# Kernel tuning notes

Measured on AMD Instinct MI355X. Metric: run time of the kernel, lower is better.

The kernel has to match this reference:

```python
import jax, jax.numpy as jnp
import numpy as np

N, G, P = 512, 11560, 2000
E_SG, E_GP, E_PP = 1000000, 200000, 50000
HID, HEADS, L = 192, 4, 2
C = HID // HEADS
NQ, OUT = 20, 128
EPS = 1e-5


def setup_inputs():
    key = jax.random.key(0)
    ks = iter(jax.random.split(key, 64))
    def rn(shape, s=0.05):
        return jax.random.normal(next(ks), shape, jnp.float32) * s
    def ri(n, hi):
        return jax.random.randint(next(ks), (n,), 0, hi)
    return dict(
        x_sample=rn((N, HID), 1.0), x_gene=rn((G, HID), 1.0), x_pathway=rn((P, HID), 1.0),
        e_sg_src=ri(E_SG, N), e_sg_dst=ri(E_SG, G),
        e_gp_src=ri(E_GP, G), e_gp_dst=ri(E_GP, P),
        e_pp_src=ri(E_PP, P), e_pp_dst=ri(E_PP, P),
        sage_Wl=rn((L, 2, HID, HID)), sage_bl=jnp.zeros((L, 2, HID)), sage_Wr=rn((L, 2, HID, HID)),
        gat_Wl=rn((L, 3, HID, HID)), gat_bl=jnp.zeros((L, 3, HID)),
        gat_Wr=rn((L, 3, HID, HID)), gat_br=jnp.zeros((L, 3, HID)),
        gat_att=rn((L, 3, HEADS, C), 0.1), gat_bias=jnp.zeros((L, 3, HID)),
        ln_g=jnp.ones((L, 3, HID)), ln_b=jnp.zeros((L, 3, HID)),
        pool_query=rn((NQ, HID), 1.0),
        pool_in_w=rn((3 * HID, HID)), pool_in_b=jnp.zeros((3 * HID,)),
        pool_out_w=rn((HID, HID)), pool_out_b=jnp.zeros((HID,)),
        ff_w1=rn((HID, HID)), ff_b1=jnp.zeros((HID,)),
        ff_w2=rn((HID, HID)), ff_b2=jnp.zeros((HID,)),
        pool_ln_g=jnp.ones((HID,)), pool_ln_b=jnp.zeros((HID,)),
        proj_w=rn((OUT, HID)), proj_b=jnp.zeros((OUT,)),
    )


def _ln(x, g, b):
    mu = x.mean(-1, keepdims=True)
    v = ((x - mu) ** 2).mean(-1, keepdims=True)
    return (x - mu) / jnp.sqrt(v + EPS) * g + b


def _sage(x_src, x_dst, src, dst, Wl, bl, Wr, n_dst):
    # PyG SAGEConv: lin_l(mean_aggr(x_src[neighbors])) + lin_r(x_dst)
    s = jax.ops.segment_sum(x_src[src], dst, num_segments=n_dst)
    cnt = jax.ops.segment_sum(jnp.ones((src.shape[0],), x_src.dtype), dst, num_segments=n_dst)
    mean = s / jnp.maximum(cnt, 1.0)[:, None]
    return mean @ Wl.T + bl + x_dst @ Wr.T


def _gatv2(x_src, x_dst, src, dst, Wl, bl, Wr, br, att, bias, n_dst):
    # transform nodes first (cheap), then gather per edge
    gl = (x_src @ Wl.T + bl).reshape(-1, HEADS, C)[src]   # [E,H,C]
    gr = (x_dst @ Wr.T + br).reshape(-1, HEADS, C)[dst]   # [E,H,C]
    e = jax.nn.leaky_relu(gl + gr, 0.2)
    score = jnp.einsum('ehc,hc->eh', e, att)              # [E,H]
    m = jax.ops.segment_max(score, dst, num_segments=n_dst)
    ex = jnp.exp(score - m[dst])
    den = jax.ops.segment_sum(ex, dst, num_segments=n_dst)
    alpha = ex / (den[dst] + 1e-16)
    out = jax.ops.segment_sum(alpha[:, :, None] * gl, dst, num_segments=n_dst)
    return out.reshape(n_dst, HID) + bias


def reference(x_sample, x_gene, x_pathway, e_sg_src, e_sg_dst, e_gp_src, e_gp_dst,
              e_pp_src, e_pp_dst, sage_Wl, sage_bl, sage_Wr, gat_Wl, gat_bl, gat_Wr,
              gat_br, gat_att, gat_bias, ln_g, ln_b, pool_query, pool_in_w, pool_in_b,
              pool_out_w, pool_out_b, ff_w1, ff_b1, ff_w2, ff_b2, pool_ln_g, pool_ln_b,
              proj_w, proj_b):
    xs, xg, xp = x_sample, x_gene, x_pathway
    for l in range(L):
        og = _sage(xs, xg, e_sg_src, e_sg_dst, sage_Wl[l, 0], sage_bl[l, 0], sage_Wr[l, 0], G)
        os_ = _sage(xg, xs, e_sg_dst, e_sg_src, sage_Wl[l, 1], sage_bl[l, 1], sage_Wr[l, 1], N)
        op = _gatv2(xg, xp, e_gp_src, e_gp_dst, gat_Wl[l, 0], gat_bl[l, 0], gat_Wr[l, 0],
                    gat_br[l, 0], gat_att[l, 0], gat_bias[l, 0], P)
        og = og + _gatv2(xp, xg, e_gp_dst, e_gp_src, gat_Wl[l, 1], gat_bl[l, 1], gat_Wr[l, 1],
                         gat_br[l, 1], gat_att[l, 1], gat_bias[l, 1], G)
        op = op + _gatv2(xp, xp, e_pp_src, e_pp_dst, gat_Wl[l, 2], gat_bl[l, 2], gat_Wr[l, 2],
                         gat_br[l, 2], gat_att[l, 2], gat_bias[l, 2], P)
        # residual + LayerNorm (dropout = identity in eval)
        xs = _ln(xs + os_, ln_g[l, 0], ln_b[l, 0])
        xg = _ln(xg + og, ln_g[l, 1], ln_b[l, 1])
        xp = _ln(xp + op, ln_g[l, 2], ln_b[l, 2])
    # MultiQueryPooling over sample nodes (batch=1 MultiheadAttention)
    Wq, Wk, Wv = jnp.split(pool_in_w, 3, axis=0)
    bq, bk, bv = jnp.split(pool_in_b, 3, axis=0)
    q = (pool_query @ Wq.T + bq).reshape(NQ, HEADS, C)
    k = (xs @ Wk.T + bk).reshape(N, HEADS, C)
    v = (xs @ Wv.T + bv).reshape(N, HEADS, C)
    attn = jax.nn.softmax(jnp.einsum('qhc,nhc->hqn', q, k) / (C ** 0.5), axis=-1)
    o = jnp.einsum('hqn,nhc->qhc', attn, v).reshape(NQ, HID) @ pool_out_w.T + pool_out_b
    pooled = o.mean(0)  # [HID]
    h = jax.nn.relu(pooled @ ff_w1.T + ff_b1) @ ff_w2.T + ff_b2
    h = _ln(h, pool_ln_g, pool_ln_b)
    return (h @ proj_w.T + proj_b)[None, :]  # [1, OUT]
```

## Files before the change

### kernel.cpp

```cpp
#include <hip/hip_runtime.h>

#define N_S 512
#define N_G 11560
#define N_P 2000
#define NE_SG 1000000
#define NE_GP 200000
#define NE_PP 50000
#define HID 192
#define HEADS 4
#define CDIM 48
#define NQd 20
#define OUTD 128
#define LDK 12288
#define SPLITK 16
#define CHUNKK 768

typedef __attribute__((ext_vector_type(8))) short short8;
typedef __attribute__((ext_vector_type(4))) float float4v;

__device__ __forceinline__ float bf2f(unsigned short u){
  union { unsigned int i; float f; } x; x.i = ((unsigned int)u) << 16; return x.f;
}
__device__ __forceinline__ unsigned short f2bf(float f){
  union { float f; unsigned int i; } u; u.f = f;
  unsigned int r = u.i + 0x7FFFu + ((u.i >> 16) & 1u);
  return (unsigned short)(r >> 16);
}
__device__ __forceinline__ ushort4 f4bf(float4 v){
  return make_ushort4(f2bf(v.x), f2bf(v.y), f2bf(v.z), f2bf(v.w));
}

__global__ __launch_bounds__(256) void k_detect(const unsigned int* __restrict__ raw,
                                                int* __restrict__ flag){
  __shared__ int cnt;
  if (threadIdx.x == 0) cnt = 0;
  __syncthreads();
  int c = 0;
  for (int i = threadIdx.x; i < 2048; i += 256) {
    float f = __uint_as_float(raw[i]);
    float a = fabsf(f);
    if (f == f && a > 1e-4f && a < 1000.0f) c++;
  }
  atomicAdd(&cnt, c);
  __syncthreads();
  if (threadIdx.x == 0) flag[0] = (cnt >= 1024) ? 1 : 0;
}

#define NLOAD 27
#define LOADBX 2048
struct LoadDesc { const void* src; float* dst; int n; };
struct LoadTable { LoadDesc d[NLOAD]; };
__global__ __launch_bounds__(256)
void k_load_all(LoadTable tab, const int* __restrict__ flag){
  LoadDesc de = tab.d[blockIdx.y];
  int fp32 = flag[0];
  for (int i = blockIdx.x*256 + threadIdx.x; i < de.n; i += LOADBX*256) {
    if (fp32) de.dst[i] = ((const float*)de.src)[i];
    else      de.dst[i] = bf2f(((const unsigned short*)de.src)[i]);
  }
}

__global__ __launch_bounds__(256)
void k_cntbuild(const int* __restrict__ src, const int* __restrict__ dst,
                int* __restrict__ cg, int E){
  int i = blockIdx.x*256 + threadIdx.x;
  if (i >= E) return;
  atomicAdd(&cg[(size_t)dst[i]*N_S + src[i]], 1);
}

__global__ __launch_bounds__(256)
void k_cvtT(const int* __restrict__ cg, unsigned short* __restrict__ bfA,
            unsigned short* __restrict__ bfB){
  __shared__ unsigned short tile[64][68];
  int g0 = blockIdx.x*64, s0 = blockIdx.y*64;
  int t = threadIdx.x; int r = t>>2, seg = t&3;
  int g = g0 + r;
  if (g < N_G) {
    const int* row = cg + (size_t)g*N_S + s0 + seg*16;
    unsigned short* arow = bfA + (size_t)g*N_S + s0 + seg*16;
    #pragma unroll
    for (int i=0;i<16;i++){
      unsigned short v = f2bf((float)row[i]);
      tile[r][seg*16+i] = v;
      arow[i] = v;
    }
  } else {
    #pragma unroll
    for (int i=0;i<16;i++) tile[r][seg*16+i] = 0;
  }
  __syncthreads();
  int s = s0 + r;
  unsigned short* brow = bfB + (size_t)s*LDK + g0 + seg*16;
  #pragma unroll
  for (int i=0;i<16;i++) brow[i] = tile[seg*16+i][r];
}

__global__ __launch_bounds__(256)
void k_rowinv_i(const int* __restrict__ A, int lda, int cols, int n,
                float* __restrict__ outp){
  int row = blockIdx.x*4 + (threadIdx.x >> 6);
  if (row >= n) return;
  int lane = threadIdx.x & 63;
  const int* Ar = A + (size_t)row*lda;
  float s = 0.0f;
  for (int c = lane; c < cols; c += 64) s += (float)Ar[c];
  #pragma unroll
  for (int o = 32; o; o >>= 1) s += __shfl_xor(s, o);
  if (lane == 0) outp[row] = 1.0f / fmaxf(s, 1.0f);
}
__global__ __launch_bounds__(256)
void k_rowinv_h(const unsigned short* __restrict__ A, int lda, int cols, int n,
                float* __restrict__ outp){
  int row = blockIdx.x;
  if (row >= n) return;
  int t = threadIdx.x;
  const short8* Av = (const short8*)(A + (size_t)row*lda);
  float s = 0.0f;
  for (int i = t; i < cols/8; i += 256) {
    short8 v = Av[i];
    #pragma unroll
    for (int j = 0; j < 8; j++) s += bf2f((unsigned short)v[j]);
  }
  #pragma unroll
  for (int o = 32; o; o >>= 1) s += __shfl_xor(s, o);
  __shared__ float red[4];
  int w = t >> 6, lane = t & 63;
  if (lane == 0) red[w] = s;
  __syncthreads();
  if (t == 0) {
    float tot = red[0] + red[1] + red[2] + red[3];
    outp[row] = 1.0f / fmaxf(tot, 1.0f);
  }
}

struct TransJobs { const float* inA; unsigned short* outA; int nA; int ldoA; int rbA;
                   const float* inB; unsigned short* outB; int nB; int ldoB; };
__global__ __launch_bounds__(256)
void k_transpose2(TransJobs tj){
  const float* in; unsigned short* outp; int n, ldo, r0;
  int bx = blockIdx.x;
  if (bx < tj.rbA) { in = tj.inA; outp = tj.outA; n = tj.nA; ldo = tj.ldoA; r0 = bx*64; }
  else             { in = tj.inB; outp = tj.outB; n = tj.nB; ldo = tj.ldoB; r0 = (bx - tj.rbA)*64; }
  __shared__ float tile[64][65];
  int c0 = blockIdx.y*64;
  int t = threadIdx.x;
  int r = t >> 2, seg = t & 3;
  int grr = r0 + r;
  if (grr < n) {
    #pragma unroll
    for (int i = 0; i < 4; i++) {
      float4 v = *(const float4*)(in + (size_t)grr*HID + c0 + seg*16 + i*4);
      tile[r][seg*16+i*4+0] = v.x; tile[r][seg*16+i*4+1] = v.y;
      tile[r][seg*16+i*4+2] = v.z; tile[r][seg*16+i*4+3] = v.w;
    }
  } else {
    #pragma unroll
    for (int i = 0; i < 16; i++) tile[r][seg*16+i] = 0.0f;
  }
  __syncthreads();
  int w = t >> 6, lane = t & 63;
  if (r0 + lane < ldo) {
    #pragma unroll
    for (int j = 0; j < 16; j++) {
      int c = w*16 + j;
      outp[(size_t)(c0+c)*ldo + r0 + lane] = f2bf(tile[lane][c]);
    }
  }
}

struct CsrJob { const int* src; const int* dst; int E; int n;
                int* deg; int* rowptr; int* cursor; int* col; };
struct CsrJobs { CsrJob j[3]; };

__global__ __launch_bounds__(256) void k_hist3(CsrJobs jobs){
  CsrJob jb = jobs.j[blockIdx.y];
  int i = blockIdx.x*256 + threadIdx.x;
  if (i < jb.E) atomicAdd(&jb.deg[jb.dst[i]], 1);
}
__global__ __launch_bounds__(256) void k_scan3(CsrJobs jobs){
  CsrJob jb = jobs.j[blockIdx.x];
  __shared__ int part[256];
  __shared__ int pre[256];
  int t = threadIdx.x;
  int n = jb.n;
  int C = (n + 255) >> 8;
  int lo = t*C, hi = min(n, lo + C);
  int s = 0;
  for (int i = lo; i < hi; i++) s += jb.deg[i];
  part[t] = s;
  __syncthreads();
  if (t == 0) {
    int acc = 0;
    for (int i = 0; i < 256; i++) { pre[i] = acc; acc += part[i]; }
    jb.rowptr[n] = acc;
  }
  __syncthreads();
  int run = pre[t];
  for (int i = lo; i < hi; i++) {
    jb.rowptr[i] = run; jb.cursor[i] = run; run += jb.deg[i];
  }
}
__global__ __launch_bounds__(256) void k_fill3(CsrJobs jobs){
  CsrJob jb = jobs.j[blockIdx.y];
  int i = blockIdx.x*256 + threadIdx.x;
  if (i >= jb.E) return;
  int pos = atomicAdd(&jb.cursor[jb.dst[i]], 1);
  jb.col[pos] = jb.src[i];
}

#define LDA 200
__global__ __launch_bounds__(256)
void k_gemm(const float* __restrict__ A,
            const float* __restrict__ W, const float* __restrict__ bias,
            float* __restrict__ outp, int n)
{
  __shared__ __align__(16) unsigned short Asm[64*LDA];
  __shared__ __align__(16) unsigned short Wsm[64*LDA];
  int t = threadIdx.x;
  int row0 = blockIdx.x * 64;
  int col0 = blockIdx.y * 64;
  {
    int r = t >> 2, seg = t & 3;
    int gr = row0 + r;
    unsigned short* ad = Asm + r*LDA + seg*48;
    if (gr < n) {
      const float* Ar = A + (size_t)gr*HID + seg*48;
      #pragma unroll
      for (int i = 0; i < 12; i++) {
        float4 v = *reinterpret_cast<const float4*>(Ar + i*4);
        *reinterpret_cast<ushort4*>(ad + i*4) = f4bf(v);
      }
    } else {
      ushort4 z = make_ushort4(0,0,0,0);
      #pragma unroll
      for (int i = 0; i < 12; i++) *reinterpret_cast<ushort4*>(ad + i*4) = z;
    }
    const float* Wr = W + (size_t)(col0 + r)*HID + seg*48;
    unsigned short* wd = Wsm + r*LDA + seg*48;
    #pragma unroll
    for (int i = 0; i < 12; i++) {
      float4 v = *reinterpret_cast<const float4*>(Wr + i*4);
      *reinterpret_cast<ushort4*>(wd + i*4) = f4bf(v);
    }
  }
  __syncthreads();
  int w = t >> 6, lane = t & 63;
  int quad = lane >> 4, mr = lane & 15;
  float4v acc[4] = {};
  const unsigned short* Abase = Asm + (w*16 + mr)*LDA + quad*8;
  const unsigned short* Wbase = Wsm + mr*LDA + quad*8;
  #pragma unroll
  for (int k0 = 0; k0 < 6; k0++) {
    short8 a = *reinterpret_cast<const short8*>(Abase + k0*32);
    #pragma unroll
    for (int ct = 0; ct < 4; ct++) {
      short8 b = *reinterpret_cast<const short8*>(Wbase + ct*16*LDA + k0*32);
      acc[ct] = __builtin_amdgcn_mfma_f32_16x16x32_bf16(a, b, acc[ct], 0, 0, 0);
    }
  }
  #pragma unroll
  for (int ct = 0; ct < 4; ct++) {
    #pragma unroll
    for (int reg = 0; reg < 4; reg++) {
      int rr = row0 + w*16 + quad*4 + reg;
      if (rr < n) {
        int cc = col0 + ct*16 + mr;
        outp[(size_t)rr*HID + cc] = acc[ct][reg] + bias[cc];
      }
    }
  }
}

struct GemmJob { const float* A; const float* W; const float* bias;
                 unsigned short* out; int n; };
struct GemmJobs { GemmJob j[6]; int rb[7]; };
__global__ __launch_bounds__(256)
void k_gemm6(GemmJobs jobs)
{
  int bx = blockIdx.x;
  int z = 0;
  #pragma unroll
  for (int q = 1; q < 6; q++) if (bx >= jobs.rb[q]) z = q;
  GemmJob jb = jobs.j[z];
  int row0 = (bx - jobs.rb[z]) * 64;
  __shared__ __align__(16) unsigned short Asm[64*LDA];
  __shared__ __align__(16) unsigned short Wsm[64*LDA];
  int t = threadIdx.x;
  int col0 = blockIdx.y * 64;
  {
    int r = t >> 2, seg = t & 3;
    int gr = row0 + r;
    unsigned short* ad = Asm + r*LDA + seg*48;
    if (gr < jb.n) {
      const float* Ar = jb.A + (size_t)gr*HID + seg*48;
      #pragma unroll
      for (int i = 0; i < 12; i++) {
        float4 v = *reinterpret_cast<const float4*>(Ar + i*4);
        *reinterpret_cast<ushort4*>(ad + i*4) = f4bf(v);
      }
    } else {
      ushort4 zz = make_ushort4(0,0,0,0);
      #pragma unroll
      for (int i = 0; i < 12; i++) *reinterpret_cast<ushort4*>(ad + i*4) = zz;
    }
    const float* Wr = jb.W + (size_t)(col0 + r)*HID + seg*48;
    unsigned short* wd = Wsm + r*LDA + seg*48;
    #pragma unroll
    for (int i = 0; i < 12; i++) {
      float4 v = *reinterpret_cast<const float4*>(Wr + i*4);
      *reinterpret_cast<ushort4*>(wd + i*4) = f4bf(v);
    }
  }
  __syncthreads();
  int w = t >> 6, lane = t & 63;
  int quad = lane >> 4, mr = lane & 15;
  float4v acc[4] = {};
  const unsigned short* Abase = Asm + (w*16 + mr)*LDA + quad*8;
  const unsigned short* Wbase = Wsm + mr*LDA + quad*8;
  #pragma unroll
  for (int k0 = 0; k0 < 6; k0++) {
    short8 a = *reinterpret_cast<const short8*>(Abase + k0*32);
    #pragma unroll
    for (int ct = 0; ct < 4; ct++) {
      short8 b = *reinterpret_cast<const short8*>(Wbase + ct*16*LDA + k0*32);
      acc[ct] = __builtin_amdgcn_mfma_f32_16x16x32_bf16(a, b, acc[ct], 0, 0, 0);
    }
  }
  #pragma unroll
  for (int ct = 0; ct < 4; ct++) {
    #pragma unroll
    for (int reg = 0; reg < 4; reg++) {
      int rr = row0 + w*16 + quad*4 + reg;
      if (rr < jb.n) {
        int cc = col0 + ct*16 + mr;
        jb.out[(size_t)rr*HID + cc] = f2bf(acc[ct][reg] + jb.bias[cc]);
      }
    }
  }
}

struct PoolJob { const float* A; const float* W; const float* bias;
                 float* out; int n; };
struct PoolJobs { PoolJob j[3]; int rb[4]; };
__global__ __launch_bounds__(256)
void k_gemm3(PoolJobs jobs)
{
  int bx = blockIdx.x;
  int z = 0;
  if (bx >= jobs.rb[1]) z = 1;
  if (bx >= jobs.rb[2]) z = 2;
  PoolJob jb = jobs.j[z];
  int row0 = (bx - jobs.rb[z]) * 64;
  __shared__ __align__(16) unsigned short Asm[64*LDA];
  __shared__ __align__(16) unsigned short Wsm[64*LDA];
  int t = threadIdx.x;
  int col0 = blockIdx.y * 64;
  {
    int r = t >> 2, seg = t & 3;
    int gr = row0 + r;
    unsigned short* ad = Asm + r*LDA + seg*48;
    if (gr < jb.n) {
      const float* Ar = jb.A + (size_t)gr*HID + seg*48;
      #pragma unroll
      for (int i = 0; i < 12; i++) {
        float4 v = *reinterpret_cast<const float4*>(Ar + i*4);
        *reinterpret_cast<ushort4*>(ad + i*4) = f4bf(v);
      }
    } else {
      ushort4 zz = make_ushort4(0,0,0,0);
      #pragma unroll
      for (int i = 0; i < 12; i++) *reinterpret_cast<ushort4*>(ad + i*4) = zz;
    }
    const float* Wr = jb.W + (size_t)(col0 + r)*HID + seg*48;
    unsigned short* wd = Wsm + r*LDA + seg*48;
    #pragma unroll
    for (int i = 0; i < 12; i++) {
      float4 v = *reinterpret_cast<const float4*>(Wr + i*4);
      *reinterpret_cast<ushort4*>(wd + i*4) = f4bf(v);
    }
  }
  __syncthreads();
  int w = t >> 6, lane = t & 63;
  int quad = lane >> 4, mr = lane & 15;
  float4v acc[4] = {};
  const unsigned short* Abase = Asm + (w*16 + mr)*LDA + quad*8;
  const unsigned short* Wbase = Wsm + mr*LDA + quad*8;
  #pragma unroll
  for (int k0 = 0; k0 < 6; k0++) {
    short8 a = *reinterpret_cast<const short8*>(Abase + k0*32);
    #pragma unroll
    for (int ct = 0; ct < 4; ct++) {
      short8 b = *reinterpret_cast<const short8*>(Wbase + ct*16*LDA + k0*32);
      acc[ct] = __builtin_amdgcn_mfma_f32_16x16x32_bf16(a, b, acc[ct], 0, 0, 0);
    }
  }
  #pragma unroll
  for (int ct = 0; ct < 4; ct++) {
    #pragma unroll
    for (int reg = 0; reg < 4; reg++) {
      int rr = row0 + w*16 + quad*4 + reg;
      if (rr < jb.n) {
        int cc = col0 + ct*16 + mr;
        jb.out[(size_t)rr*HID + cc] = acc[ct][reg] + jb.bias[cc];
      }
    }
  }
}

struct G2Job { const float* A1; const float* rs1; const float* W1;
               const float* A2; const float* W2; const float* bias;
               float* out; int n; };
struct G2Jobs { G2Job j[2]; int rb[3]; };
__global__ __launch_bounds__(256)
void k_gemm2(G2Jobs jobs)
{
  int bx = blockIdx.x;
  int z = (bx >= jobs.rb[1]) ? 1 : 0;
  G2Job jb = jobs.j[z];
  int row0 = (bx - jobs.rb[z]) * 64;
  __shared__ __align__(16) unsigned short Asm[64*LDA];
  __shared__ __align__(16) unsigned short Wsm[64*LDA];
  int t = threadIdx.x;
  int col0 = blockIdx.y * 64;
  int r = t >> 2, seg = t & 3;
  int w = t >> 6, lane = t & 63;
  int quad = lane >> 4, mr = lane & 15;
  float4v acc[4] = {};
  for (int p = 0; p < 2; p++) {
    if (p) __syncthreads();
    const float* A = p ? jb.A2 : jb.A1;
    const float* W = p ? jb.W2 : jb.W1;
    {
      int gr = row0 + r;
      unsigned short* ad = Asm + r*LDA + seg*48;
      if (gr < jb.n) {
        float sc = (!p && jb.rs1) ? jb.rs1[gr] : 1.0f;
        const float* Ar = A + (size_t)gr*HID + seg*48;
        #pragma unroll
        for (int i = 0; i < 12; i++) {
          float4 v = *reinterpret_cast<const float4*>(Ar + i*4);
          v.x *= sc; v.y *= sc; v.z *= sc; v.w *= sc;
          *reinterpret_cast<ushort4*>(ad + i*4) = f4bf(v);
        }
      } else {
        ushort4 zz = make_ushort4(0,0,0,0);
        #pragma unroll
        for (int i = 0; i < 12; i++) *reinterpret_cast<ushort4*>(ad + i*4) = zz;
      }
      const float* Wr = W + (size_t)(col0 + r)*HID + seg*48;
      unsigned short* wd = Wsm + r*LDA + seg*48;
      #pragma unroll
      for (int i = 0; i < 12; i++) {
        float4 v = *reinterpret_cast<const float4*>(Wr + i*4);
        *reinterpret_cast<ushort4*>(wd + i*4) = f4bf(v);
      }
    }
    __syncthreads();
    const unsigned short* Abase = Asm + (w*16 + mr)*LDA + quad*8;
    const unsigned short* Wbase = Wsm + mr*LDA + quad*8;
    #pragma unroll
    for (int k0 = 0; k0 < 6; k0++) {
      short8 a = *reinterpret_cast<const short8*>(Abase + k0*32);
      #pragma unroll
      for (int ct = 0; ct < 4; ct++) {
        short8 b = *reinterpret_cast<const short8*>(Wbase + ct*16*LDA + k0*32);
        acc[ct] = __builtin_amdgcn_mfma_f32_16x16x32_bf16(a, b, acc[ct], 0, 0, 0);
      }
    }
  }
  #pragma unroll
  for (int ct = 0; ct < 4; ct++) {
    #pragma unroll
    for (int reg = 0; reg < 4; reg++) {
      int rr = row0 + w*16 + quad*4 + reg;
      if (rr < jb.n) {
        int cc = col0 + ct*16 + mr;
        jb.out[(size_t)rr*HID + cc] = acc[ct][reg] + jb.bias[cc];
      }
    }
  }
}

#define BKG 128
#define LDG 136
struct KJob { const unsigned short* A; int lda;
              const unsigned short* W; int ldw;
              float* out; int n; int kbeg; int kend; };
struct KJobs { KJob j[17]; int rb[18]; };
__global__ __launch_bounds__(256)
void k_gemm_k(KJobs jobs)
{
  int bx = blockIdx.x;
  int z = 0;
  for (int q = 1; q < 17; q++) if (bx >= jobs.rb[q]) z = q;
  KJob jb = jobs.j[z];
  int row0 = (bx - jobs.rb[z]) * 64;
  __shared__ __align__(16) unsigned short Asm[64*LDG];
  __shared__ __align__(16) unsigned short Wsm[64*LDG];
  int t = threadIdx.x;
  int col0 = blockIdx.y * 64;
  int r = t >> 2, seg = t & 3;
  int w = t >> 6, lane = t & 63;
  int quad = lane >> 4, mr = lane & 15;
  float4v acc[4] = {};
  for (int k0 = jb.kbeg; k0 < jb.kend; k0 += BKG) {
    {
      int gr = row0 + r;
      unsigned short* ad = Asm + r*LDG + seg*32;
      if (gr < jb.n) {
        const unsigned short* Ar = jb.A + (size_t)gr*jb.lda + k0 + seg*32;
        #pragma unroll
        for (int i = 0; i < 4; i++) *(uint4*)(ad + i*8) = *(const uint4*)(Ar + i*8);
      } else {
        uint4 zz = make_uint4(0,0,0,0);
        #pragma unroll
        for (int i = 0; i < 4; i++) *(uint4*)(ad + i*8) = zz;
      }
      const unsigned short* Wr = jb.W + (size_t)(col0 + r)*jb.ldw + k0 + seg*32;
      unsigned short* wd = Wsm + r*LDG + seg*32;
      #pragma unroll
      for (int i = 0; i < 4; i++) *(uint4*)(wd + i*8) = *(const uint4*)(Wr + i*8);
    }
    __syncthreads();
    const unsigned short* Abase = Asm + (w*16 + mr)*LDG + quad*8;
    const unsigned short* Wbase = Wsm + mr*LDG + quad*8;
    #pragma unroll
    for (int kk = 0; kk < 4; kk++) {
      short8 a = *(const short8*)(Abase + kk*32);
      #pragma unroll
      for (int ct = 0; ct < 4; ct++) {
        short8 b = *(const short8*)(Wbase + ct*16*LDG + kk*32);
        acc[ct] = __builtin_amdgcn_mfma_f32_16x16x32_bf16(a, b, acc[ct], 0, 0, 0);
      }
    }
    __syncthreads();
  }
  #pragma unroll
  for (int ct = 0; ct < 4; ct++) {
    #pragma unroll
    for (int reg = 0; reg < 4; reg++) {
      int rr = row0 + w*16 + quad*4 + reg;
      if (rr < jb.n) jb.out[(size_t)rr*HID + col0 + ct*16 + mr] = acc[ct][reg];
    }
  }
}

__global__ __launch_bounds__(256)
void k_reduce_sk(const float* __restrict__ part, float* __restrict__ outp, int n){
  int i = blockIdx.x*256 + threadIdx.x;
  if (i >= n*HID) return;
  float s = 0.0f;
  #pragma unroll
  for (int z = 0; z < SPLITK; z++) s += part[(size_t)z*n*HID + i];
  outp[i] = s;
}

struct GatJob { const unsigned short* gl; const unsigned short* gr;
                const int* rowptr; const int* col;
                const float* att; const float* bias; float* out; int ndst; int accum; };
struct GatJobs { GatJob j[3]; int bo[4]; };

#define GLS_LD 200
__global__ __launch_bounds__(256)
void k_gat_all(GatJobs jobs)
{
  int bx = blockIdx.x;
  int jz = 0;
  if (bx >= jobs.bo[1]) jz = 1;
  if (bx >= jobs.bo[2]) jz = 2;
  GatJob jb = jobs.j[jz];
  int tid = threadIdx.x;
  int w = tid >> 6, lane = tid & 63;
  int dst = (bx - jobs.bo[jz])*4 + w;
  bool active = dst < jb.ndst;
  __shared__ float attS[HID];
  __shared__ float grS[4][HID];
  __shared__ __align__(16) unsigned short glS[4][16][GLS_LD];
  __shared__ float swS[4][4][16];
  __shared__ float fS[4][4];
  __shared__ float lS[4][4];
  if (tid < HID) attS[tid] = jb.att[tid];
  if (active) {
    const unsigned short* grr = jb.gr + (size_t)dst*HID;
    grS[w][lane]     = bf2f(grr[lane]);
    grS[w][lane+64]  = bf2f(grr[lane+64]);
    grS[w][lane+128] = bf2f(grr[lane+128]);
  }
  __syncthreads();
  if (!active) return;

  int h16 = lane >> 4, j16 = lane & 15;
  int start = jb.rowptr[dst], end = jb.rowptr[dst+1];
  float m = -1e30f, l = 0.0f;
  float acc0 = 0.f, acc1 = 0.f, acc2 = 0.f;
  int hd0 = lane/48, hd1 = (lane+64)/48, hd2 = (lane+128)/48;
  const float* attH = attS + h16*CDIM;
  const float* grH  = grS[w] + h16*CDIM;

  for (int c0 = start; c0 < end; c0 += 16) {
    int nc = min(16, end - c0);
    float sc = -1e30f;
    if (j16 < nc) {
      int s = jb.col[c0 + j16];
      const short8* glv = (const short8*)(jb.gl + (size_t)s*HID + h16*CDIM);
      unsigned short* ls = &glS[w][j16][h16*CDIM];
      float a = 0.0f;
      #pragma unroll
      for (int v8 = 0; v8 < 6; v8++) {
        short8 g8 = glv[v8];
        *(short8*)(ls + v8*8) = g8;
        #pragma unroll
        for (int jj = 0; jj < 8; jj++) {
          float v = bf2f((unsigned short)g8[jj]) + grH[v8*8+jj];
          v = v > 0.0f ? v : 0.2f*v;
          a += v * attH[v8*8+jj];
        }
      }
      sc = a;
    }
    float cm = sc;
    cm = fmaxf(cm, __shfl_xor(cm, 1));
    cm = fmaxf(cm, __shfl_xor(cm, 2));
    cm = fmaxf(cm, __shfl_xor(cm, 4));
    cm = fmaxf(cm, __shfl_xor(cm, 8));
    float nm = fmaxf(m, cm);
    float f = __expf(m - nm);
    l *= f;
    float e = (j16 < nc) ? __expf(sc - nm) : 0.0f;
    swS[w][h16][j16] = e;
    float cl = e;
    cl += __shfl_xor(cl, 1);
    cl += __shfl_xor(cl, 2);
    cl += __shfl_xor(cl, 4);
    cl += __shfl_xor(cl, 8);
    l += cl;
    m = nm;
    if (j16 == 0) fS[w][h16] = f;
    acc0 *= fS[w][hd0]; acc1 *= fS[w][hd1]; acc2 *= fS[w][hd2];
    for (int j = 0; j < nc; j++) {
      acc0 += swS[w][hd0][j] * bf2f(glS[w][j][lane]);
      acc1 += swS[w][hd1][j] * bf2f(glS[w][j][lane+64]);
      acc2 += swS[w][hd2][j] * bf2f(glS[w][j][lane+128]);
    }
  }
  if (j16 == 0) lS[w][h16] = l;
  float* od = jb.out + (size_t)dst*HID;
  float v0 = acc0 / (lS[w][hd0] + 1e-16f) + jb.bias[lane];
  float v1 = acc1 / (lS[w][hd1] + 1e-16f) + jb.bias[lane+64];
  float v2 = acc2 / (lS[w][hd2] + 1e-16f) + jb.bias[lane+128];
  if (jb.accum) { v0 += od[lane]; v1 += od[lane+64]; v2 += od[lane+128]; }
  od[lane] = v0; od[lane+64] = v1; od[lane+128] = v2;
}

__global__ __launch_bounds__(64)
void k_ln3(float* __restrict__ xs, const float* __restrict__ osb,
           float* __restrict__ xg, const float* __restrict__ og,
           float* __restrict__ xp, const float* __restrict__ opb,
           const float* __restrict__ op2,
           const float* __restrict__ LNg, const float* __restrict__ LNb, int l)
{
  int r = blockIdx.x;
  float* x; const float* d1; const float* d2 = nullptr; int typ;
  if (r < N_S)            { x = xs + (size_t)r*HID; d1 = osb + (size_t)r*HID; typ = 0; }
  else if (r < N_S + N_G) { int rr = r - N_S; x = xg + (size_t)rr*HID; d1 = og + (size_t)rr*HID; typ = 1; }
  else                    { int rr = r - N_S - N_G; x = xp + (size_t)rr*HID; d1 = opb + (size_t)rr*HID;
                            d2 = op2 + (size_t)rr*HID; typ = 2; }
  const float* g = LNg + (l*3 + typ)*HID;
  const float* b = LNb + (l*3 + typ)*HID;
  int lane = threadIdx.x;
  float v[3]; float sum = 0.0f;
  #pragma unroll
  for (int j=0;j<3;j++){
    int d = j*64 + lane;
    float t = x[d] + d1[d];
    if (d2) t += d2[d];
    v[j] = t; sum += t;
  }
  #pragma unroll
  for (int o=32;o;o>>=1) sum += __shfl_xor(sum, o);
  float mu = sum * (1.0f/HID);
  float var = 0.0f;
  #pragma unroll
  for (int j=0;j<3;j++){ float dd = v[j]-mu; var += dd*dd; }
  #pragma unroll
  for (int o=32;o;o>>=1) var += __shfl_xor(var, o);
  var *= (1.0f/HID);
  float inv = rsqrtf(var + 1e-5f);
  #pragma unroll
  for (int j=0;j<3;j++){
    int d = j*64 + lane;
    x[d] = (v[j]-mu)*inv*g[d] + b[d];
  }
}

__global__ __launch_bounds__(256)
void k_pool_attn(const float* __restrict__ qb, const float* __restrict__ kb,
                 const float* __restrict__ vb, float* __restrict__ ob)
{
  int h = blockIdx.x & 3;
  int q = blockIdx.x >> 2;
  __shared__ float prob[N_S];
  __shared__ float red[256];
  int t = threadIdx.x;
  const float* qrow = qb + (size_t)q*HID + h*CDIM;
  const float scale = 0.14433756729740643f;
  for (int n = t; n < N_S; n += 256) {
    const float* krow = kb + (size_t)n*HID + h*CDIM;
    float s = 0.0f;
    #pragma unroll 8
    for (int c=0;c<CDIM;c++) s += qrow[c]*krow[c];
    prob[n] = s * scale;
  }
  __syncthreads();
  float m = -1e30f;
  for (int n=t;n<N_S;n+=256) m = fmaxf(m, prob[n]);
  red[t] = m; __syncthreads();
  for (int s2=128;s2;s2>>=1){ if (t<s2) red[t]=fmaxf(red[t],red[t+s2]); __syncthreads(); }
  m = red[0]; __syncthreads();
  float sum = 0.0f;
  for (int n=t;n<N_S;n+=256){ float e=__expf(prob[n]-m); prob[n]=e; sum+=e; }
  red[t] = sum; __syncthreads();
  for (int s2=128;s2;s2>>=1){ if (t<s2) red[t]+=red[t+s2]; __syncthreads(); }
  float inv = 1.0f/red[0];
  __syncthreads();
  if (t < CDIM) {
    float acc = 0.0f;
    for (int n=0;n<N_S;n++) acc += prob[n]*vb[(size_t)n*HID + h*CDIM + t];
    ob[(size_t)q*HID + h*CDIM + t] = acc * inv;
  }
}

__global__ __launch_bounds__(192)
void k_tail(const float* __restrict__ ob2,
            const float* ffw1, const float* ffb1,
            const float* ffw2, const float* ffb2,
            const float* lng, const float* lnb,
            const float* pw, const float* pb,
            void* __restrict__ outp, const int* __restrict__ flag)
{
  __shared__ float pooled[HID];
  __shared__ float hh[HID];
  __shared__ float stats[2];
  int t = threadIdx.x;
  float a = 0.0f;
  for (int q=0;q<NQd;q++) a += ob2[q*HID + t];
  pooled[t] = a * (1.0f/NQd);
  __syncthreads();
  float s1 = ffb1[t];
  for (int k=0;k<HID;k++) s1 += pooled[k]*ffw1[t*HID+k];
  hh[t] = fmaxf(s1, 0.0f);
  __syncthreads();
  float s2 = ffb2[t];
  for (int k=0;k<HID;k++) s2 += hh[k]*ffw2[t*HID+k];
  __syncthreads();
  hh[t] = s2;
  __syncthreads();
  if (t == 0) {
    float mu=0.0f; for (int k=0;k<HID;k++) mu += hh[k];
    mu *= (1.0f/HID);
    float v=0.0f; for (int k=0;k<HID;k++){ float d=hh[k]-mu; v+=d*d; }
    v *= (1.0f/HID);
    stats[0]=mu; stats[1]=rsqrtf(v + 1e-5f);
  }
  __syncthreads();
  pooled[t] = (hh[t]-stats[0])*stats[1]*lng[t] + lnb[t];
  __syncthreads();
  if (t < OUTD) {
    float acc = pb[t];
    for (int k=0;k<HID;k++) acc += pooled[k]*pw[t*HID+k];
    if (flag[0]) ((float*)outp)[t] = acc;
    else         ((unsigned short*)outp)[t] = f2bf(acc);
  }
}

extern "C" void kernel_launch(void* const* d_in, const int* in_sizes, int n_in,
                              void* d_out, int out_size, void* d_ws, size_t ws_size,
                              hipStream_t stream)
{
  const int* sg_src = (const int*)d_in[3];
  const int* sg_dst = (const int*)d_in[4];
  const int* gp_src = (const int*)d_in[5];
  const int* gp_dst = (const int*)d_in[6];
  const int* pp_src = (const int*)d_in[7];
  const int* pp_dst = (const int*)d_in[8];

  float* base = (float*)d_ws;
  size_t off = 0;
  auto alloc = [&](size_t nf){ nf = (nf + 3) & ~(size_t)3; float* p = base + off; off += nf; return p; };
  int*   flag = (int*)alloc(4);
  float* xs   = alloc((size_t)N_S*HID);
  float* xg   = alloc((size_t)N_G*HID);
  float* xp   = alloc((size_t)N_P*HID);
  float* qin  = alloc((size_t)NQd*HID);
  float* Wsl  = alloc(2*2*HID*HID); float* bsl = alloc(2*2*HID); float* Wsr = alloc(2*2*HID*HID);
  float* Wgl  = alloc(2*3*HID*HID); float* bgl = alloc(2*3*HID);
  float* Wgr  = alloc(2*3*HID*HID); float* bgr = alloc(2*3*HID);
  float* Agat = alloc(2*3*HEADS*CDIM); float* Bgat = alloc(2*3*HID);
  float* LNg  = alloc(2*3*HID); float* LNb = alloc(2*3*HID);
  float* Pinw = alloc(3*HID*HID); float* Pinb = alloc(3*HID);
  float* Poutw= alloc(HID*HID);   float* Poutb= alloc(HID);
  float* Fw1  = alloc(HID*HID);   float* Fb1  = alloc(HID);
  float* Fw2  = alloc(HID*HID);   float* Fb2  = alloc(HID);
  float* PLg  = alloc(HID);       float* PLb  = alloc(HID);
  float* Pw   = alloc(OUTD*HID);  float* Pb   = alloc(OUTD);
  float* agg  = alloc((size_t)N_G*HID);
  float* aggS = alloc((size_t)N_S*HID);
  float* og   = alloc((size_t)N_G*HID);
  float* osb  = alloc((size_t)N_S*HID);
  float* opb  = alloc((size_t)N_P*HID);
  float* op2  = alloc((size_t)N_P*HID);
  unsigned short* glGb  = (unsigned short*)alloc((size_t)N_G*HID/2);
  unsigned short* grGb  = (unsigned short*)alloc((size_t)N_G*HID/2);
  unsigned short* grP0b = (unsigned short*)alloc((size_t)N_P*HID/2);
  unsigned short* glP1b = (unsigned short*)alloc((size_t)N_P*HID/2);
  unsigned short* glP2b = (unsigned short*)alloc((size_t)N_P*HID/2);
  unsigned short* grP2b = (unsigned short*)alloc((size_t)N_P*HID/2);
  float* qbuf = alloc((size_t)NQd*HID);
  float* kbuf = alloc((size_t)N_S*HID);
  float* vbuf = alloc((size_t)N_S*HID);
  float* obuf = alloc((size_t)NQd*HID);
  float* ob2  = alloc((size_t)NQd*HID);
  int*            CntGi = (int*)alloc((size_t)N_G*N_S);
  unsigned short* CntGb = (unsigned short*)alloc((size_t)N_G*N_S/2);
  unsigned short* CntSb = (unsigned short*)alloc((size_t)N_S*LDK/2);
  unsigned short* xsTb  = (unsigned short*)alloc((size_t)HID*N_S/2);
  unsigned short* xgTb  = (unsigned short*)alloc((size_t)HID*LDK/2);
  float* part = alloc((size_t)SPLITK*N_S*HID);
  float* invdegG = alloc(N_G);
  float* invdegS = alloc(N_S);
  int* degAll = (int*)alloc(2*N_P + N_G + 4);
  int* curAll = (int*)alloc(2*N_P + N_G + 4);
  int* rp_gp_p = (int*)alloc(N_P+2);  int* col_gp_p = (int*)alloc(NE_GP);
  int* rp_gp_g = (int*)alloc(N_G+2);  int* col_gp_g = (int*)alloc(NE_GP);
  int* rp_pp_p = (int*)alloc(N_P+2);  int* col_pp_p = (int*)alloc(NE_PP);
  (void)ws_size; (void)in_sizes; (void)n_in; (void)out_size;

  k_detect<<<1,256,0,stream>>>((const unsigned int*)d_in[0], flag);

  {
    LoadTable tab;
    int k = 0;
    auto add = [&](int i, float* dst, int n){ tab.d[k].src = d_in[i]; tab.d[k].dst = dst; tab.d[k].n = n; k++; };
    add(0,  xs,  N_S*HID);  add(1,  xg,  N_G*HID);  add(2,  xp,  N_P*HID);
    add(9,  Wsl, 2*2*HID*HID); add(10, bsl, 2*2*HID); add(11, Wsr, 2*2*HID*HID);
    add(12, Wgl, 2*3*HID*HID); add(13, bgl, 2*3*HID);
    add(14, Wgr, 2*3*HID*HID); add(15, bgr, 2*3*HID);
    add(16, Agat, 2*3*HEADS*CDIM); add(17, Bgat, 2*3*HID);
    add(18, LNg, 2*3*HID); add(19, LNb, 2*3*HID);
    add(20, qin, NQd*HID);
    add(21, Pinw, 3*HID*HID); add(22, Pinb, 3*HID);
    add(23, Poutw, HID*HID);  add(24, Poutb, HID);
    add(25, Fw1, HID*HID); add(26, Fb1, HID);
    add(27, Fw2, HID*HID); add(28, Fb2, HID);
    add(29, PLg, HID); add(30, PLb, HID);
    add(31, Pw, OUTD*HID); add(32, Pb, OUTD);
    k_load_all<<<dim3(LOADBX, NLOAD),256,0,stream>>>(tab, flag);
  }

  hipMemsetAsync(CntGi, 0, (size_t)N_G*N_S*4, stream);
  hipMemsetAsync(degAll, 0, (size_t)(2*N_P + N_G)*4, stream);
  k_cntbuild<<<(NE_SG+255)/256,256,0,stream>>>(sg_src, sg_dst, CntGi, NE_SG);
  k_cvtT<<<dim3(LDK/64, N_S/64),256,0,stream>>>(CntGi, CntGb, CntSb);
  k_rowinv_i<<<(N_G+3)/4,256,0,stream>>>(CntGi, N_S, N_S, N_G, invdegG);
  k_rowinv_h<<<N_S,256,0,stream>>>(CntSb, LDK, LDK, N_S, invdegS);

  {
    CsrJobs jobs;
    jobs.j[0] = { gp_src, gp_dst, NE_GP, N_P, degAll,           rp_gp_p, curAll,           col_gp_p };
    jobs.j[1] = { gp_dst, gp_src, NE_GP, N_G, degAll+N_P,       rp_gp_g, curAll+N_P,       col_gp_g };
    jobs.j[2] = { pp_src, pp_dst, NE_PP, N_P, degAll+N_P+N_G,   rp_pp_p, curAll+N_P+N_G,   col_pp_p };
    k_hist3<<<dim3((NE_GP+255)/256, 3),256,0,stream>>>(jobs);
    k_scan3<<<3,256,0,stream>>>(jobs);
    k_fill3<<<dim3((NE_GP+255)/256, 3),256,0,stream>>>(jobs);
  }

  const int RB_G = (N_G+63)/64, RB_P = (N_P+63)/64;
  const int GB_P = (N_P+3)/4,  GB_G = (N_G+3)/4;

  for (int l=0; l<2; l++) {
    {
      TransJobs tj;
      tj.inA = xs; tj.outA = xsTb; tj.nA = N_S; tj.ldoA = N_S; tj.rbA = 8;
      tj.inB = xg; tj.outB = xgTb; tj.nB = N_G; tj.ldoB = LDK;
      k_transpose2<<<dim3(8 + LDK/64, 3),256,0,stream>>>(tj);
    }
    {
      KJobs kj;
      kj.j[0] = { CntGb, N_S, xsTb, N_S, agg, N_G, 0, N_S };
      kj.rb[0] = 0; kj.rb[1] = RB_G;
      for (int z = 0; z < SPLITK; z++) {
        kj.j[1+z] = { CntSb, LDK, xgTb, LDK, part + (size_t)z*N_S*HID, N_S,
                      z*CHUNKK, (z+1)*CHUNKK };
        kj.rb[2+z] = kj.rb[1+z] + 8;
      }
      k_gemm_k<<<dim3(kj.rb[17],3),256,0,stream>>>(kj);
    }
    k_reduce_sk<<<(N_S*HID+255)/256,256,0,stream>>>(part, aggS, N_S);
    {
      G2Jobs g2;
      g2.j[0] = { agg,  invdegG, Wsl + (size_t)(l*2+0)*HID*HID,
                  xg, Wsr + (size_t)(l*2+0)*HID*HID, bsl + (l*2+0)*HID, og,  N_G };
      g2.j[1] = { aggS, invdegS, Wsl + (size_t)(l*2+1)*HID*HID,
                  xs, Wsr + (size_t)(l*2+1)*HID*HID, bsl + (l*2+1)*HID, osb, N_S };
      g2.rb[0] = 0; g2.rb[1] = RB_G; g2.rb[2] = RB_G + (N_S+63)/64;
      k_gemm2<<<dim3(g2.rb[2],3),256,0,stream>>>(g2);
    }
    {
      GemmJobs gj;
      int w0 = l*3+0, w1 = l*3+1, w2 = l*3+2;
      gj.j[0] = { xg, Wgl + (size_t)w0*HID*HID, bgl + w0*HID, glGb,  N_G };
      gj.j[1] = { xp, Wgr + (size_t)w0*HID*HID, bgr + w0*HID, grP0b, N_P };
      gj.j[2] = { xp, Wgl + (size_t)w1*HID*HID, bgl + w1*HID, glP1b, N_P };
      gj.j[3] = { xg, Wgr + (size_t)w1*HID*HID, bgr + w1*HID, grGb,  N_G };
      gj.j[4] = { xp, Wgl + (size_t)w2*HID*HID, bgl + w2*HID, glP2b, N_P };
      gj.j[5] = { xp, Wgr + (size_t)w2*HID*HID, bgr + w2*HID, grP2b, N_P };
      int nrb[6] = { RB_G, RB_P, RB_P, RB_G, RB_P, RB_P };
      gj.rb[0] = 0;
      for (int q = 0; q < 6; q++) gj.rb[q+1] = gj.rb[q] + nrb[q];
      k_gemm6<<<dim3(gj.rb[6],3),256,0,stream>>>(gj);
    }
    {
      GatJobs gt;
      int w0 = l*3+0, w1 = l*3+1, w2 = l*3+2;
      gt.j[0] = { glGb,  grP0b, rp_gp_p, col_gp_p, Agat + (size_t)w0*HID, Bgat + (size_t)w0*HID, opb, N_P, 0 };
      gt.j[1] = { glP1b, grGb,  rp_gp_g, col_gp_g, Agat + (size_t)w1*HID, Bgat + (size_t)w1*HID, og,  N_G, 1 };
      gt.j[2] = { glP2b, grP2b, rp_pp_p, col_pp_p, Agat + (size_t)w2*HID, Bgat + (size_t)w2*HID, op2, N_P, 0 };
      gt.bo[0] = 0; gt.bo[1] = GB_P; gt.bo[2] = GB_P + GB_G; gt.bo[3] = GB_P + GB_G + GB_P;
      k_gat_all<<<dim3(gt.bo[3]),256,0,stream>>>(gt);
    }
    k_ln3<<<N_S+N_G+N_P,64,0,stream>>>(xs, osb, xg, og, xp, opb, op2, LNg, LNb, l);
  }

  {
    PoolJobs pj;
    pj.j[0] = { qin, Pinw,                     Pinb,         qbuf, NQd };
    pj.j[1] = { xs,  Pinw + (size_t)HID*HID,   Pinb + HID,   kbuf, N_S };
    pj.j[2] = { xs,  Pinw + (size_t)2*HID*HID, Pinb + 2*HID, vbuf, N_S };
    pj.rb[0] = 0; pj.rb[1] = 1; pj.rb[2] = 1 + (N_S+63)/64; pj.rb[3] = pj.rb[2] + (N_S+63)/64;
    k_gemm3<<<dim3(pj.rb[3],3),256,0,stream>>>(pj);
  }
  k_pool_attn<<<NQd*HEADS,256,0,stream>>>(qbuf, kbuf, vbuf, obuf);
  k_gemm<<<dim3(1,3),256,0,stream>>>(obuf, Poutw, Poutb, ob2, NQd);
  k_tail<<<1,HID,0,stream>>>(ob2, Fw1, Fb1, Fw2, Fb2, PLg, PLb, Pw, Pb, d_out, flag);
}
```

Measured before the change: 638.3 us.

## Keep bf16 shadow copies of node features and vectorize GAT aggregation

The loader and LayerNorm kernels now also write bf16 copies of the node features. The GEMM kernels then read these directly with 16-byte loads instead of loading fp32 and converting on every use, which cuts global read traffic and conversion work in the repeated GEMMs. Separately, the GAT aggregation now has 48 lanes each handle 4 contiguous channels with float4 accumulators and vector loads, replacing 3 strided scalar accumulators per lane. The cost is extra bf16 writes and memory, and a quarter of the lanes sit idle during aggregation.

Measured after the change: 613.0 us. 1.04x faster.

```diff
diff --git a/kernel.cpp b/kernel.cpp
--- a/kernel.cpp
+++ b/kernel.cpp
@@ -48,15 +48,17 @@
 
 #define NLOAD 27
 #define LOADBX 2048
-struct LoadDesc { const void* src; float* dst; int n; };
+struct LoadDesc { const void* src; float* dst; unsigned short* dst16; int n; };
 struct LoadTable { LoadDesc d[NLOAD]; };
 __global__ __launch_bounds__(256)
 void k_load_all(LoadTable tab, const int* __restrict__ flag){
   LoadDesc de = tab.d[blockIdx.y];
   int fp32 = flag[0];
+  unsigned short* m = de.dst16;
   for (int i = blockIdx.x*256 + threadIdx.x; i < de.n; i += LOADBX*256) {
-    if (fp32) de.dst[i] = ((const float*)de.src)[i];
-    else      de.dst[i] = bf2f(((const unsigned short*)de.src)[i]);
+    float v = fp32 ? ((const float*)de.src)[i] : bf2f(((const unsigned short*)de.src)[i]);
+    de.dst[i] = v;
+    if (m) m[i] = f2bf(v);
   }
 }
 
@@ -271,7 +273,7 @@
   }
 }
 
-struct GemmJob { const float* A; const float* W; const float* bias;
+struct GemmJob { const unsigned short* A; const float* W; const float* bias;
                  unsigned short* out; int n; };
 struct GemmJobs { GemmJob j[6]; int rb[7]; };
 __global__ __launch_bounds__(256)
@@ -292,16 +294,13 @@
     int gr = row0 + r;
     unsigned short* ad = Asm + r*LDA + seg*48;
     if (gr < jb.n) {
-      const float* Ar = jb.A + (size_t)gr*HID + seg*48;
-      #pragma unroll
-      for (int i = 0; i < 12; i++) {
-        float4 v = *reinterpret_cast<const float4*>(Ar + i*4);
-        *reinterpret_cast<ushort4*>(ad + i*4) = f4bf(v);
-      }
+      const unsigned short* Ar = jb.A + (size_t)gr*HID + seg*48;
+      #pragma unroll
+      for (int i = 0; i < 6; i++) *(uint4*)(ad + i*8) = *(const uint4*)(Ar + i*8);
     } else {
-      ushort4 zz = make_ushort4(0,0,0,0);
-      #pragma unroll
-      for (int i = 0; i < 12; i++) *reinterpret_cast<ushort4*>(ad + i*4) = zz;
+      uint4 zz = make_uint4(0,0,0,0);
+      #pragma unroll
+      for (int i = 0; i < 6; i++) *(uint4*)(ad + i*8) = zz;
     }
     const float* Wr = jb.W + (size_t)(col0 + r)*HID + seg*48;
     unsigned short* wd = Wsm + r*LDA + seg*48;
@@ -339,7 +338,7 @@
   }
 }
 
-struct PoolJob { const float* A; const float* W; const float* bias;
+struct PoolJob { const unsigned short* A; const float* W; const float* bias;
                  float* out; int n; };
 struct PoolJobs { PoolJob j[3]; int rb[4]; };
 __global__ __launch_bounds__(256)
@@ -360,16 +359,13 @@
     int gr = row0 + r;
     unsigned short* ad = Asm + r*LDA + seg*48;
     if (gr < jb.n) {
-      const float* Ar = jb.A + (size_t)gr*HID + seg*48;
-      #pragma unroll
-      for (int i = 0; i < 12; i++) {
-        float4 v = *reinterpret_cast<const float4*>(Ar + i*4);
-        *reinterpret_cast<ushort4*>(ad + i*4) = f4bf(v);
-      }
+      const unsigned short* Ar = jb.A + (size_t)gr*HID + seg*48;
+      #pragma unroll
+      for (int i = 0; i < 6; i++) *(uint4*)(ad + i*8) = *(const uint4*)(Ar + i*8);
     } else {
-      ushort4 zz = make_ushort4(0,0,0,0);
-      #pragma unroll
-      for (int i = 0; i < 12; i++) *reinterpret_cast<ushort4*>(ad + i*4) = zz;
+      uint4 zz = make_uint4(0,0,0,0);
+      #pragma unroll
+      for (int i = 0; i < 6; i++) *(uint4*)(ad + i*8) = zz;
     }
     const float* Wr = jb.W + (size_t)(col0 + r)*HID + seg*48;
     unsigned short* wd = Wsm + r*LDA + seg*48;
@@ -408,7 +404,7 @@
 }
 
 struct G2Job { const float* A1; const float* rs1; const float* W1;
-               const float* A2; const float* W2; const float* bias;
+               const unsigned short* A2; const float* W2; const float* bias;
                float* out; int n; };
 struct G2Jobs { G2Job j[2]; int rb[3]; };
 __global__ __launch_bounds__(256)
@@ -428,24 +424,29 @@
   float4v acc[4] = {};
   for (int p = 0; p < 2; p++) {
     if (p) __syncthreads();
-    const float* A = p ? jb.A2 : jb.A1;
     const float* W = p ? jb.W2 : jb.W1;
     {
       int gr = row0 + r;
       unsigned short* ad = Asm + r*LDA + seg*48;
       if (gr < jb.n) {
-        float sc = (!p && jb.rs1) ? jb.rs1[gr] : 1.0f;
-        const float* Ar = A + (size_t)gr*HID + seg*48;
-        #pragma unroll
-        for (int i = 0; i < 12; i++) {
-          float4 v = *reinterpret_cast<const float4*>(Ar + i*4);
-          v.x *= sc; v.y *= sc; v.z *= sc; v.w *= sc;
-          *reinterpret_cast<ushort4*>(ad + i*4) = f4bf(v);
+        if (p == 0) {
+          float sc = jb.rs1 ? jb.rs1[gr] : 1.0f;
+          const float* Ar = jb.A1 + (size_t)gr*HID + seg*48;
+          #pragma unroll
+          for (int i = 0; i < 12; i++) {
+            float4 v = *reinterpret_cast<const float4*>(Ar + i*4);
+            v.x *= sc; v.y *= sc; v.z *= sc; v.w *= sc;
+            *reinterpret_cast<ushort4*>(ad + i*4) = f4bf(v);
+          }
+        } else {
+          const unsigned short* Ar = jb.A2 + (size_t)gr*HID + seg*48;
+          #pragma unroll
+          for (int i = 0; i < 6; i++) *(uint4*)(ad + i*8) = *(const uint4*)(Ar + i*8);
         }
       } else {
-        ushort4 zz = make_ushort4(0,0,0,0);
+        uint4 zz = make_uint4(0,0,0,0);
         #pragma unroll
-        for (int i = 0; i < 12; i++) *reinterpret_cast<ushort4*>(ad + i*4) = zz;
+        for (int i = 0; i < 6; i++) *(uint4*)(ad + i*8) = zz;
       }
       const float* Wr = W + (size_t)(col0 + r)*HID + seg*48;
       unsigned short* wd = Wsm + r*LDA + seg*48;
@@ -590,10 +591,12 @@
   if (!active) return;
 
   int h16 = lane >> 4, j16 = lane & 15;
+  bool aggL = lane < 48;
+  int hAgg = lane / 12;
+  if (hAgg > 3) hAgg = 3;
   int start = jb.rowptr[dst], end = jb.rowptr[dst+1];
   float m = -1e30f, l = 0.0f;
-  float acc0 = 0.f, acc1 = 0.f, acc2 = 0.f;
-  int hd0 = lane/48, hd1 = (lane+64)/48, hd2 = (lane+128)/48;
+  float4 facc = make_float4(0.f, 0.f, 0.f, 0.f);
   const float* attH = attS + h16*CDIM;
   const float* grH  = grS[w] + h16*CDIM;
 
@@ -636,20 +639,35 @@
     l += cl;
     m = nm;
     if (j16 == 0) fS[w][h16] = f;
-    acc0 *= fS[w][hd0]; acc1 *= fS[w][hd1]; acc2 *= fS[w][hd2];
-    for (int j = 0; j < nc; j++) {
-      acc0 += swS[w][hd0][j] * bf2f(glS[w][j][lane]);
-      acc1 += swS[w][hd1][j] * bf2f(glS[w][j][lane+64]);
-      acc2 += swS[w][hd2][j] * bf2f(glS[w][j][lane+128]);
+    if (aggL) {
+      float fr = fS[w][hAgg];
+      facc.x *= fr; facc.y *= fr; facc.z *= fr; facc.w *= fr;
+      for (int j = 0; j < nc; j++) {
+        float wgt = swS[w][hAgg][j];
+        uint2 u = *(const uint2*)&glS[w][j][lane*4];
+        facc.x += wgt * __uint_as_float(u.x << 16);
+        facc.y += wgt * __uint_as_float(u.x & 0xffff0000u);
+        facc.z += wgt * __uint_as_float(u.y << 16);
+        facc.w += wgt * __uint_as_float(u.y & 0xffff0000u);
+      }
     }
   }
   if (j16 == 0) lS[w][h16] = l;
-  float* od = jb.out + (size_t)dst*HID;
-  float v0 = acc0 / (lS[w][hd0] + 1e-16f) + jb.bias[lane];
-  float v1 = acc1 / (lS[w][hd1] + 1e-16f) + jb.bias[lane+64];
-  float v2 = acc2 / (lS[w][hd2] + 1e-16f) + jb.bias[lane+128];
-  if (jb.accum) { v0 += od[lane]; v1 += od[lane+64]; v2 += od[lane+128]; }
-  od[lane] = v0; od[lane+64] = v1; od[lane+128] = v2;
+  if (aggL) {
+    float invl = 1.0f / (lS[w][hAgg] + 1e-16f);
+    float4 bi = *(const float4*)(jb.bias + lane*4);
+    float4 o;
+    o.x = facc.x*invl + bi.x;
+    o.y = facc.y*invl + bi.y;
+    o.z = facc.z*invl + bi.z;
+    o.w = facc.w*invl + bi.w;
+    float* od = jb.out + (size_t)dst*HID;
+    if (jb.accum) {
+      float4 pv = *(const float4*)(od + lane*4);
+      o.x += pv.x; o.y += pv.y; o.z += pv.z; o.w += pv.w;
+    }
+    *(float4*)(od + lane*4) = o;
+  }
 }
 
 __global__ __launch_bounds__(64)
@@ -657,14 +675,18 @@
            float* __restrict__ xg, const float* __restrict__ og,
            float* __restrict__ xp, const float* __restrict__ opb,
            const float* __restrict__ op2,
+           unsigned short* __restrict__ xsb, unsigned short* __restrict__ xgb,
+           unsigned short* __restrict__ xpb,
            const float* __restrict__ LNg, const float* __restrict__ LNb, int l)
 {
   int r = blockIdx.x;
-  float* x; const float* d1; const float* d2 = nullptr; int typ;
-  if (r < N_S)            { x = xs + (size_t)r*HID; d1 = osb + (size_t)r*HID; typ = 0; }
-  else if (r < N_S + N_G) { int rr = r - N_S; x = xg + (size_t)rr*HID; d1 = og + (size_t)rr*HID; typ = 1; }
+  float* x; const float* d1; const float* d2 = nullptr; unsigned short* xb; int typ;
+  if (r < N_S)            { x = xs + (size_t)r*HID; d1 = osb + (size_t)r*HID;
+                            xb = xsb + (size_t)r*HID; typ = 0; }
+  else if (r < N_S + N_G) { int rr = r - N_S; x = xg + (size_t)rr*HID; d1 = og + (size_t)rr*HID;
+                            xb = xgb + (size_t)rr*HID; typ = 1; }
   else                    { int rr = r - N_S - N_G; x = xp + (size_t)rr*HID; d1 = opb + (size_t)rr*HID;
-                            d2 = op2 + (size_t)rr*HID; typ = 2; }
+                            d2 = op2 + (size_t)rr*HID; xb = xpb + (size_t)rr*HID; typ = 2; }
   const float* g = LNg + (l*3 + typ)*HID;
   const float* b = LNb + (l*3 + typ)*HID;
   int lane = threadIdx.x;
@@ -689,7 +711,9 @@
   #pragma unroll
   for (int j=0;j<3;j++){
     int d = j*64 + lane;
-    x[d] = (v[j]-mu)*inv*g[d] + b[d];
+    float val = (v[j]-mu)*inv*g[d] + b[d];
+    x[d] = val;
+    xb[d] = f2bf(val);
   }
 }
 
@@ -809,6 +833,10 @@
   float* osb  = alloc((size_t)N_S*HID);
   float* opb  = alloc((size_t)N_P*HID);
   float* op2  = alloc((size_t)N_P*HID);
+  unsigned short* xsb  = (unsigned short*)alloc((size_t)N_S*HID/2);
+  unsigned short* xgb  = (unsigned short*)alloc((size_t)N_G*HID/2);
+  unsigned short* xpb  = (unsigned short*)alloc((size_t)N_P*HID/2);
+  unsigned short* qinb = (unsigned short*)alloc((size_t)NQd*HID/2 + 4);
   unsigned short* glGb  = (unsigned short*)alloc((size_t)N_G*HID/2);
   unsigned short* grGb  = (unsigned short*)alloc((size_t)N_G*HID/2);
   unsigned short* grP0b = (unsigned short*)alloc((size_t)N_P*HID/2);
@@ -840,20 +868,21 @@
   {
     LoadTable tab;
     int k = 0;
-    auto add = [&](int i, float* dst, int n){ tab.d[k].src = d_in[i]; tab.d[k].dst = dst; tab.d[k].n = n; k++; };
-    add(0,  xs,  N_S*HID);  add(1,  xg,  N_G*HID);  add(2,  xp,  N_P*HID);
-    add(9,  Wsl, 2*2*HID*HID); add(10, bsl, 2*2*HID); add(11, Wsr, 2*2*HID*HID);
-    add(12, Wgl, 2*3*HID*HID); add(13, bgl, 2*3*HID);
-    add(14, Wgr, 2*3*HID*HID); add(15, bgr, 2*3*HID);
-    add(16, Agat, 2*3*HEADS*CDIM); add(17, Bgat, 2*3*HID);
-    add(18, LNg, 2*3*HID); add(19, LNb, 2*3*HID);
-    add(20, qin, NQd*HID);
-    add(21, Pinw, 3*HID*HID); add(22, Pinb, 3*HID);
-    add(23, Poutw, HID*HID);  add(24, Poutb, HID);
-    add(25, Fw1, HID*HID); add(26, Fb1, HID);
-    add(27, Fw2, HID*HID); add(28, Fb2, HID);
-    add(29, PLg, HID); add(30, PLb, HID);
-    add(31, Pw, OUTD*HID); add(32, Pb, OUTD);
+    auto add = [&](int i, float* dst, unsigned short* m, int n){
+      tab.d[k].src = d_in[i]; tab.d[k].dst = dst; tab.d[k].dst16 = m; tab.d[k].n = n; k++; };
+    add(0,  xs, xsb, N_S*HID);  add(1,  xg, xgb, N_G*HID);  add(2,  xp, xpb, N_P*HID);
+    add(9,  Wsl, nullptr, 2*2*HID*HID); add(10, bsl, nullptr, 2*2*HID); add(11, Wsr, nullptr, 2*2*HID*HID);
+    add(12, Wgl, nullptr, 2*3*HID*HID); add(13, bgl, nullptr, 2*3*HID);
+    add(14, Wgr, nullptr, 2*3*HID*HID); add(15, bgr, nullptr, 2*3*HID);
+    add(16, Agat, nullptr, 2*3*HEADS*CDIM); add(17, Bgat, nullptr, 2*3*HID);
+    add(18, LNg, nullptr, 2*3*HID); add(19, LNb, nullptr, 2*3*HID);
+    add(20, qin, qinb, NQd*HID);
+    add(21, Pinw, nullptr, 3*HID*HID); add(22, Pinb, nullptr, 3*HID);
+    add(23, Poutw, nullptr, HID*HID);  add(24, Poutb, nullptr, HID);
+    add(25, Fw1, nullptr, HID*HID); add(26, Fb1, nullptr, HID);
+    add(27, Fw2, nullptr, HID*HID); add(28, Fb2, nullptr, HID);
+    add(29, PLg, nullptr, HID); add(30, PLb, nullptr, HID);
+    add(31, Pw, nullptr, OUTD*HID); add(32, Pb, nullptr, OUTD);
     k_load_all<<<dim3(LOADBX, NLOAD),256,0,stream>>>(tab, flag);
   }
 
@@ -899,21 +928,21 @@
     {
       G2Jobs g2;
       g2.j[0] = { agg,  invdegG, Wsl + (size_t)(l*2+0)*HID*HID,
-                  xg, Wsr + (size_t)(l*2+0)*HID*HID, bsl + (l*2+0)*HID, og,  N_G };
+                  xgb, Wsr + (size_t)(l*2+0)*HID*HID, bsl + (l*2+0)*HID, og,  N_G };
       g2.j[1] = { aggS, invdegS, Wsl + (size_t)(l*2+1)*HID*HID,
-                  xs, Wsr + (size_t)(l*2+1)*HID*HID, bsl + (l*2+1)*HID, osb, N_S };
+                  xsb, Wsr + (size_t)(l*2+1)*HID*HID, bsl + (l*2+1)*HID, osb, N_S };
       g2.rb[0] = 0; g2.rb[1] = RB_G; g2.rb[2] = RB_G + (N_S+63)/64;
       k_gemm2<<<dim3(g2.rb[2],3),256,0,stream>>>(g2);
     }
     {
       GemmJobs gj;
       int w0 = l*3+0, w1 = l*3+1, w2 = l*3+2;
-      gj.j[0] = { xg, Wgl + (size_t)w0*HID*HID, bgl + w0*HID, glGb,  N_G };
-      gj.j[1] = { xp, Wgr + (size_t)w0*HID*HID, bgr + w0*HID, grP0b, N_P };
-      gj.j[2] = { xp, Wgl + (size_t)w1*HID*HID, bgl + w1*HID, glP1b, N_P };
-      gj.j[3] = { xg, Wgr + (size_t)w1*HID*HID, bgr + w1*HID, grGb,  N_G };
-      gj.j[4] = { xp, Wgl + (size_t)w2*HID*HID, bgl + w2*HID, glP2b, N_P };
-      gj.j[5] = { xp, Wgr + (size_t)w2*HID*HID, bgr + w2*HID, grP2b, N_P };
+      gj.j[0] = { xgb, Wgl + (size_t)w0*HID*HID, bgl + w0*HID, glGb,  N_G };
+      gj.j[1] = { xpb, Wgr + (size_t)w0*HID*HID, bgr + w0*HID, grP0b, N_P };
+      gj.j[2] = { xpb, Wgl + (size_t)w1*HID*HID, bgl + w1*HID, glP1b, N_P };
+      gj.j[3] = { xgb, Wgr + (size_t)w1*HID*HID, bgr + w1*HID, grGb,  N_G };
+      gj.j[4] = { xpb, Wgl + (size_t)w2*HID*HID, bgl + w2*HID, glP2b, N_P };
+      gj.j[5] = { xpb, Wgr + (size_t)w2*HID*HID, bgr + w2*HID, grP2b, N_P };
       int nrb[6] = { RB_G, RB_P, RB_P, RB_G, RB_P, RB_P };
       gj.rb[0] = 0;
       for (int q = 0; q < 6; q++) gj.rb[q+1] = gj.rb[q] + nrb[q];
@@ -928,14 +957,15 @@
       gt.bo[0] = 0; gt.bo[1] = GB_P; gt.bo[2] = GB_P + GB_G; gt.bo[3] = GB_P + GB_G + GB_P;
       k_gat_all<<<dim3(gt.bo[3]),256,0,stream>>>(gt);
     }
-    k_ln3<<<N_S+N_G+N_P,64,0,stream>>>(xs, osb, xg, og, xp, opb, op2, LNg, LNb, l);
+    k_ln3<<<N_S+N_G+N_P,64,0,stream>>>(xs, osb, xg, og, xp, opb, op2,
+                                       xsb, xgb, xpb, LNg, LNb, l);
   }
 
   {
     PoolJobs pj;
-    pj.j[0] = { qin, Pinw,                     Pinb,         qbuf, NQd };
-    pj.j[1] = { xs,  Pinw + (size_t)HID*HID,   Pinb + HID,   kbuf, N_S };
-    pj.j[2] = { xs,  Pinw + (size_t)2*HID*HID, Pinb + 2*HID, vbuf, N_S };
+    pj.j[0] = { qinb, Pinw,                     Pinb,         qbuf, NQd };
+    pj.j[1] = { xsb,  Pinw + (size_t)HID*HID,   Pinb + HID,   kbuf, N_S };
+    pj.j[2] = { xsb,  Pinw + (size_t)2*HID*HID, Pinb + 2*HID, vbuf, N_S };
     pj.rb[0] = 0; pj.rb[1] = 1; pj.rb[2] = 1 + (N_S+63)/64; pj.rb[3] = pj.rb[2] + (N_S+63)/64;
     k_gemm3<<<dim3(pj.rb[3],3),256,0,stream>>>(pj);
   }
```
